# Kernel optimization log

Hardware: AMD Instinct MI355X
Metric: run time of the kernel (lower is better)

Reference implementation:

```python
import jax, jax.numpy as jnp
import numpy as np

N, D, H = 4096, 1024, 16
DK = D // H

def setup_inputs() -> dict:
    key = jax.random.key(0)
    k1, k2 = jax.random.split(key)
    X = jax.random.normal(k1, (N, D), dtype=jnp.float32)
    # torch nn.Linear(D, 2D, bias=False): weight [2D, D]; y = x @ W.T. Store as [D, 2D].
    Wqkv = jax.random.normal(k2, (D, 2 * D), dtype=jnp.float32) * (1.0 / np.sqrt(D))
    return {"X": X, "Wqkv": Wqkv}

def reference(X, Wqkv):
    n = X.shape[0]
    proj = X @ Wqkv                      # [N, 2D]
    qk, v = jnp.split(proj, 2, axis=-1)  # each [N, D]
    qk = qk.reshape(n, H, DK)
    v = v.reshape(n, H, DK)
    scale = DK ** 0.5
    scores = jnp.einsum('nhd,mhd->hnm', qk, qk) / scale  # [H, N, N], Q == K
    att = jax.nn.softmax(scores, axis=-1)
    out = jnp.einsum('hnm,mhd->nhd', att, v)              # [N, H, DK]
    return out.reshape(n, D)
```

## Files before the change

### kernel.cpp

```cpp
#include <hip/hip_runtime.h>

typedef unsigned short u16;
typedef unsigned int u32;
typedef __bf16 bf16x8 __attribute__((ext_vector_type(8)));
typedef float f32x4 __attribute__((ext_vector_type(4)));
typedef float f32x16 __attribute__((ext_vector_type(16)));
typedef int i32x2 __attribute__((ext_vector_type(2)));
typedef unsigned int u32x4 __attribute__((ext_vector_type(4)));

#define N_TOK 4096
#define DMODEL 1024
#define NH 16
#define DKH 64

__device__ inline u16 f2bf(float f){
  unsigned u = __float_as_uint(f);
  u += 0x7fffu + ((u >> 16) & 1u);
  return (u16)(u >> 16);
}

__device__ inline float fexp2(float x){ return __builtin_amdgcn_exp2f(x); }

__global__ __launch_bounds__(256) void k_convX(const float* __restrict__ X, u16* __restrict__ Xb){
  int i = blockIdx.x*256 + threadIdx.x;
  const float4 v = reinterpret_cast<const float4*>(X)[i];
  ushort4 o; o.x=f2bf(v.x); o.y=f2bf(v.y); o.z=f2bf(v.z); o.w=f2bf(v.w);
  reinterpret_cast<ushort4*>(Xb)[i] = o;
}

__global__ __launch_bounds__(256) void k_convW(const float* __restrict__ W, u16* __restrict__ Wt){
  __shared__ float tile[64][65];
  const int bn = blockIdx.x*64;
  const int bk = blockIdx.y*64;
  const int t = threadIdx.x;
  const int c4 = (t & 15)*4;
  const int r  = t >> 4;
  #pragma unroll
  for (int i=0;i<4;i++){
    int k = r + i*16;
    const float4 v = *reinterpret_cast<const float4*>(&W[(size_t)(bk+k)*2048 + bn + c4]);
    tile[k][c4+0]=v.x; tile[k][c4+1]=v.y; tile[k][c4+2]=v.z; tile[k][c4+3]=v.w;
  }
  __syncthreads();
  #pragma unroll
  for (int i=0;i<4;i++){
    int n = r + i*16;
    ushort4 o;
    o.x = f2bf(tile[c4+0][n]);
    o.y = f2bf(tile[c4+1][n]);
    o.z = f2bf(tile[c4+2][n]);
    o.w = f2bf(tile[c4+3][n]);
    *reinterpret_cast<ushort4*>(&Wt[(size_t)(bn+n)*1024 + bk + c4]) = o;
  }
}

__global__ __launch_bounds__(256) void k_gemm(const u16* __restrict__ A, const u16* __restrict__ B,
                                              u16* __restrict__ kf_g, u16* __restrict__ vf_g){
  __shared__ alignas(16) u16 As[128*64];
  __shared__ alignas(16) u16 Bs[128*64];
  const int bm = blockIdx.y*128, bn = blockIdx.x*128;
  const int tid = threadIdx.x, wid = tid>>6, lane = tid&63;
  const int wr = wid>>1, wc = wid&1;
  const int lr = lane&15, lg = lane>>4;
  f32x4 acc[4][4] = {};

  for (int kk=0; kk<DMODEL; kk+=64){
    __syncthreads();
    #pragma unroll
    for (int i=0;i<4;i++){
      const int chunk = (wid*4+i)*64 + lane;
      const int row = chunk>>3, koc = chunk&7;
      const int swz = koc ^ (row&7);
      const u16* ga = A + (size_t)(bm+row)*DMODEL + kk + swz*8;
      const u16* gb = B + (size_t)(bn+row)*DMODEL + kk + swz*8;
      __builtin_amdgcn_global_load_lds((const __attribute__((address_space(1))) void*)ga,
          (__attribute__((address_space(3))) void*)(&As[(size_t)chunk*8]), 16, 0, 0);
      __builtin_amdgcn_global_load_lds((const __attribute__((address_space(1))) void*)gb,
          (__attribute__((address_space(3))) void*)(&Bs[(size_t)chunk*8]), 16, 0, 0);
    }
    asm volatile("s_waitcnt vmcnt(0)" ::: "memory");
    __syncthreads();
    #pragma unroll
    for (int ks=0; ks<2; ks++){
      bf16x8 af[4], bfr[4];
      #pragma unroll
      for (int m=0;m<4;m++){
        const int row = wr*64+m*16+lr, cr = ks*4+lg;
        af[m] = *reinterpret_cast<const bf16x8*>(&As[(size_t)(row*8 + (cr ^ (row&7)))*8]);
      }
      #pragma unroll
      for (int n=0;n<4;n++){
        const int row = wc*64+n*16+lr, cr = ks*4+lg;
        bfr[n] = *reinterpret_cast<const bf16x8*>(&Bs[(size_t)(row*8 + (cr ^ (row&7)))*8]);
      }
      #pragma unroll
      for (int m=0;m<4;m++)
        #pragma unroll
        for (int n=0;n<4;n++)
          acc[m][n] = __builtin_amdgcn_mfma_f32_16x16x32_bf16(af[m], bfr[n], acc[m][n], 0,0,0);
    }
  }

  #pragma unroll
  for (int m=0;m<4;m++){
    const int row0 = bm + wr*64 + m*16 + lg*4;
    #pragma unroll
    for (int n=0;n<4;n++){
      const int c = bn + wc*64 + n*16 + lr;
      if (c < DMODEL){
        const int hh = c>>6, d = c&63;
        const size_t base = ((size_t)hh*512 + (size_t)(row0>>5)*4 + (d>>4))*512;
        #pragma unroll
        for (int r=0;r<4;r++){
          const int row = row0 + r;
          kf_g[base + (size_t)(((row&31) | (((d>>3)&1)<<5)))*8 + (d&7)] = f2bf(acc[m][n][r]);
        }
      } else {
        const int cc = c - DMODEL; const int hh = cc>>6, d = cc&63;
        const size_t base = (((size_t)hh*64 + (row0>>6))*8 + (d>>5)*4 + ((row0>>4)&3))*512
                          + (size_t)(((d&31) | (((row0>>3)&1)<<5)))*8 + (row0&7);
        ushort4 o;
        o.x = f2bf(acc[m][n][0]); o.y = f2bf(acc[m][n][1]);
        o.z = f2bf(acc[m][n][2]); o.w = f2bf(acc[m][n][3]);
        *reinterpret_cast<ushort4*>(&vf_g[base]) = o;
      }
    }
  }
}

__device__ inline bf16x8 scale_bf8(bf16x8 v, float s){
  u32x4 w = __builtin_bit_cast(u32x4, v);
  u32x4 r;
  #pragma unroll
  for (int i=0;i<4;i++){
    float lo = __uint_as_float(w[i] << 16) * s;
    float hi = __uint_as_float(w[i] & 0xffff0000u) * s;
    u32 p;
    asm("v_cvt_pk_bf16_f32 %0, %1, %2" : "=v"(p) : "v"(lo), "v"(hi));
    r[i] = p;
  }
  return __builtin_bit_cast(bf16x8, r);
}

__global__ __launch_bounds__(256,3) void k_attn(const u16* __restrict__ kf_g, const u16* __restrict__ vf_g,
                                                float* __restrict__ out){
  __shared__ float comb[3][64][17];
  const int bid  = blockIdx.x;
  const int xcd  = bid & 7;
  const int slot = bid >> 3;
  const int h    = (xcd<<1) | (slot>>7);
  const int qt   = slot & 127;
  const int wid  = threadIdx.x >> 6;
  const int lane = threadIdx.x & 63;
  const int ql   = lane & 31;
  const int q0   = qt*32;
  const u16* __restrict__ Kfh = kf_g + (size_t)h*262144;
  const u16* __restrict__ Vfh = vf_g + (size_t)h*262144;
  const float SC = 0.18033688011112042f;

  bf16x8 qb[4];
  #pragma unroll
  for (int ds=0; ds<4; ds++){
    bf16x8 raw = *reinterpret_cast<const bf16x8*>(&Kfh[(size_t)((q0>>5)*4 + ds)*512 + lane*8]);
    qb[ds] = scale_bf8(raw, SC);
  }

  f32x16 o0 = {}, o1 = {};
  float lp = 0.f;
  const int kb = wid*1024;

  for (int s=0; s<32; ++s){
    const int kt = kb + s*32;
    const u16* kp = Kfh + ((size_t)(kt>>5)*4)*512 + lane*8;
    bf16x8 kf0 = *reinterpret_cast<const bf16x8*>(kp);
    bf16x8 kf1 = *reinterpret_cast<const bf16x8*>(kp + 512);
    bf16x8 kf2 = *reinterpret_cast<const bf16x8*>(kp + 1024);
    bf16x8 kf3 = *reinterpret_cast<const bf16x8*>(kp + 1536);
    const u16* vb = Vfh + ((size_t)((kt>>6)*8 + (s&1)*2))*512 + lane*8;
    bf16x8 va0 = *reinterpret_cast<const bf16x8*>(vb);
    bf16x8 va1 = *reinterpret_cast<const bf16x8*>(vb + 512);
    bf16x8 vb0 = *reinterpret_cast<const bf16x8*>(vb + 4*512);
    bf16x8 vb1 = *reinterpret_cast<const bf16x8*>(vb + 5*512);

    f32x16 p = {};
    p = __builtin_amdgcn_mfma_f32_32x32x16_bf16(kf0, qb[0], p, 0,0,0);
    p = __builtin_amdgcn_mfma_f32_32x32x16_bf16(kf1, qb[1], p, 0,0,0);
    p = __builtin_amdgcn_mfma_f32_32x32x16_bf16(kf2, qb[2], p, 0,0,0);
    p = __builtin_amdgcn_mfma_f32_32x32x16_bf16(kf3, qb[3], p, 0,0,0);

    #pragma unroll
    for (int c=0; c<16; c++) p[c] = fexp2(p[c]);
    {
      float r0 = ((p[0]+p[1])+(p[2]+p[3])) + ((p[4]+p[5])+(p[6]+p[7]));
      float r1 = ((p[8]+p[9])+(p[10]+p[11])) + ((p[12]+p[13])+(p[14]+p[15]));
      lp += r0+r1;
    }

    u32 pk[8];
    #pragma unroll
    for (int c2=0; c2<8; c2++){
      u32 a;
      asm("v_cvt_pk_bf16_f32 %0, %1, %2" : "=v"(a) : "v"(p[2*c2]), "v"(p[2*c2+1]));
      pk[c2] = a;
    }
    #pragma unroll
    for (int t2=0; t2<2; t2++){
      const int base = 4*t2;
      i32x2 r0s = __builtin_amdgcn_permlane32_swap((int)pk[base+0], (int)pk[base+2], false, false);
      i32x2 r1s = __builtin_amdgcn_permlane32_swap((int)pk[base+1], (int)pk[base+3], false, false);
      u32x4 w; w[0] = (u32)r0s[0]; w[1] = (u32)r1s[0]; w[2] = (u32)r0s[1]; w[3] = (u32)r1s[1];
      bf16x8 bt = __builtin_bit_cast(bf16x8, w);
      o0 = __builtin_amdgcn_mfma_f32_32x32x16_bf16(t2 ? va1 : va0, bt, o0, 0,0,0);
      o1 = __builtin_amdgcn_mfma_f32_32x32x16_bf16(t2 ? vb1 : vb0, bt, o1, 0,0,0);
    }
  }

  lp += __shfl_xor(lp, 32, 64);

  if (wid){
    float* c = &comb[wid-1][lane][0];
    #pragma unroll
    for (int g=0; g<16; g++) c[g] = o0[g];
    c[16] = lp;
  }
  __syncthreads();
  if (!wid){
    #pragma unroll
    for (int w=0; w<3; w++){
      const float* c = &comb[w][lane][0];
      #pragma unroll
      for (int g=0; g<16; g++) o0[g] += c[g];
      lp += c[16];
    }
  }
  __syncthreads();
  if (wid){
    float* c = &comb[wid-1][lane][0];
    #pragma unroll
    for (int g=0; g<16; g++) c[g] = o1[g];
  }
  __syncthreads();
  if (!wid){
    #pragma unroll
    for (int w=0; w<3; w++){
      const float* c = &comb[w][lane][0];
      #pragma unroll
      for (int g=0; g<16; g++) o1[g] += c[g];
    }
    const int hi = lane >> 5;
    const float inv = 1.f / lp;
    float* orow = out + (size_t)(q0 + ql)*DMODEL + h*DKH;
    #pragma unroll
    for (int g=0; g<4; g++){
      float4 s0, s1;
      s0.x = o0[4*g+0]*inv; s0.y = o0[4*g+1]*inv; s0.z = o0[4*g+2]*inv; s0.w = o0[4*g+3]*inv;
      s1.x = o1[4*g+0]*inv; s1.y = o1[4*g+1]*inv; s1.z = o1[4*g+2]*inv; s1.w = o1[4*g+3]*inv;
      *reinterpret_cast<float4*>(&orow[      8*g + 4*hi]) = s0;
      *reinterpret_cast<float4*>(&orow[32 +  8*g + 4*hi]) = s1;
    }
  }
}

extern "C" void kernel_launch(void* const* d_in, const int* in_sizes, int n_in,
                              void* d_out, int out_size, void* d_ws, size_t ws_size,
                              hipStream_t stream) {
  const float* X = (const float*)d_in[0];
  const float* W = (const float*)d_in[1];
  float* out = (float*)d_out;
  u16* Xb = (u16*)d_ws;
  u16* Wt = Xb + (size_t)N_TOK*DMODEL;
  u16* Kf = Wt + (size_t)2*DMODEL*DMODEL;
  u16* Vf = Kf + (size_t)N_TOK*DMODEL;

  k_convX<<<dim3(4096), dim3(256), 0, stream>>>(X, Xb);
  k_convW<<<dim3(32,16), dim3(256), 0, stream>>>(W, Wt);
  k_gemm <<<dim3(16,32), dim3(256), 0, stream>>>(Xb, Wt, Kf, Vf);
  k_attn <<<dim3(2048), dim3(256), 0, stream>>>(Kf, Vf, out);
}
```

Baseline: 133.4 us.

## Share K/V tiles across four query warps via double-buffered LDS staging

The attention kernel changes from splitting keys across four warps (each holding the same 32 queries, then reducing through shared memory) to giving each warp its own 32 queries. K/V tiles are loaded once per block into double-buffered LDS with global_load_lds and reused by all four warps, and the cross-warp reduction is removed. The intent is to cut global/L2 traffic for K and V by a factor of four and to overlap loads with compute. In exchange the grid shrinks to 512 blocks, occupancy drops (launch bounds 2, 64KB LDS), and two barriers per tile are added.

New measurement: 118.2 us. 1.13x faster.

```diff
diff --git a/kernel.cpp b/kernel.cpp
--- a/kernel.cpp
+++ b/kernel.cpp
@@ -142,18 +142,18 @@
   return __builtin_bit_cast(bf16x8, r);
 }
 
-__global__ __launch_bounds__(256,3) void k_attn(const u16* __restrict__ kf_g, const u16* __restrict__ vf_g,
+__global__ __launch_bounds__(256,2) void k_attn(const u16* __restrict__ kf_g, const u16* __restrict__ vf_g,
                                                 float* __restrict__ out){
-  __shared__ float comb[3][64][17];
+  __shared__ alignas(16) u16 stg[2][16384];
   const int bid  = blockIdx.x;
   const int xcd  = bid & 7;
   const int slot = bid >> 3;
-  const int h    = (xcd<<1) | (slot>>7);
-  const int qt   = slot & 127;
+  const int h    = (xcd<<1) | (slot>>5);
+  const int qt   = slot & 31;
   const int wid  = threadIdx.x >> 6;
   const int lane = threadIdx.x & 63;
   const int ql   = lane & 31;
-  const int q0   = qt*32;
+  const int q0   = qt*128 + wid*32;
   const u16* __restrict__ Kfh = kf_g + (size_t)h*262144;
   const u16* __restrict__ Vfh = vf_g + (size_t)h*262144;
   const float SC = 0.18033688011112042f;
@@ -167,97 +167,88 @@
 
   f32x16 o0 = {}, o1 = {};
   float lp = 0.f;
-  const int kb = wid*1024;
-
-  for (int s=0; s<32; ++s){
-    const int kt = kb + s*32;
-    const u16* kp = Kfh + ((size_t)(kt>>5)*4)*512 + lane*8;
-    bf16x8 kf0 = *reinterpret_cast<const bf16x8*>(kp);
-    bf16x8 kf1 = *reinterpret_cast<const bf16x8*>(kp + 512);
-    bf16x8 kf2 = *reinterpret_cast<const bf16x8*>(kp + 1024);
-    bf16x8 kf3 = *reinterpret_cast<const bf16x8*>(kp + 1536);
-    const u16* vb = Vfh + ((size_t)((kt>>6)*8 + (s&1)*2))*512 + lane*8;
-    bf16x8 va0 = *reinterpret_cast<const bf16x8*>(vb);
-    bf16x8 va1 = *reinterpret_cast<const bf16x8*>(vb + 512);
-    bf16x8 vb0 = *reinterpret_cast<const bf16x8*>(vb + 4*512);
-    bf16x8 vb1 = *reinterpret_cast<const bf16x8*>(vb + 5*512);
-
-    f32x16 p = {};
-    p = __builtin_amdgcn_mfma_f32_32x32x16_bf16(kf0, qb[0], p, 0,0,0);
-    p = __builtin_amdgcn_mfma_f32_32x32x16_bf16(kf1, qb[1], p, 0,0,0);
-    p = __builtin_amdgcn_mfma_f32_32x32x16_bf16(kf2, qb[2], p, 0,0,0);
-    p = __builtin_amdgcn_mfma_f32_32x32x16_bf16(kf3, qb[3], p, 0,0,0);
-
-    #pragma unroll
-    for (int c=0; c<16; c++) p[c] = fexp2(p[c]);
-    {
-      float r0 = ((p[0]+p[1])+(p[2]+p[3])) + ((p[4]+p[5])+(p[6]+p[7]));
-      float r1 = ((p[8]+p[9])+(p[10]+p[11])) + ((p[12]+p[13])+(p[14]+p[15]));
-      lp += r0+r1;
-    }
-
-    u32 pk[8];
-    #pragma unroll
-    for (int c2=0; c2<8; c2++){
-      u32 a;
-      asm("v_cvt_pk_bf16_f32 %0, %1, %2" : "=v"(a) : "v"(p[2*c2]), "v"(p[2*c2+1]));
-      pk[c2] = a;
-    }
-    #pragma unroll
-    for (int t2=0; t2<2; t2++){
-      const int base = 4*t2;
-      i32x2 r0s = __builtin_amdgcn_permlane32_swap((int)pk[base+0], (int)pk[base+2], false, false);
-      i32x2 r1s = __builtin_amdgcn_permlane32_swap((int)pk[base+1], (int)pk[base+3], false, false);
-      u32x4 w; w[0] = (u32)r0s[0]; w[1] = (u32)r1s[0]; w[2] = (u32)r0s[1]; w[3] = (u32)r1s[1];
-      bf16x8 bt = __builtin_bit_cast(bf16x8, w);
-      o0 = __builtin_amdgcn_mfma_f32_32x32x16_bf16(t2 ? va1 : va0, bt, o0, 0,0,0);
-      o1 = __builtin_amdgcn_mfma_f32_32x32x16_bf16(t2 ? vb1 : vb0, bt, o1, 0,0,0);
-    }
+
+  auto stage = [&](int buf, int t){
+    #pragma unroll
+    for (int i=0; i<8; i++){
+      const int c = wid + i*4;
+      const u16* src = (c < 16)
+        ? Kfh + ((size_t)(t*16 + c))*512 + lane*8
+        : Vfh + ((size_t)(t*16 + c - 16))*512 + lane*8;
+      __builtin_amdgcn_global_load_lds((const __attribute__((address_space(1))) void*)src,
+          (__attribute__((address_space(3))) void*)(&stg[buf][(size_t)c*512]), 16, 0, 0);
+    }
+  };
+
+  stage(0, 0);
+  int cur = 0;
+  for (int t=0; t<32; ++t){
+    asm volatile("s_waitcnt vmcnt(0)" ::: "memory");
+    __syncthreads();
+    if (t < 31) stage(cur^1, t+1);
+
+    const u16* kb = &stg[cur][0];
+    #pragma unroll
+    for (int ss=0; ss<4; ++ss){
+      bf16x8 kf0 = *reinterpret_cast<const bf16x8*>(&kb[(size_t)(ss*4+0)*512 + lane*8]);
+      bf16x8 kf1 = *reinterpret_cast<const bf16x8*>(&kb[(size_t)(ss*4+1)*512 + lane*8]);
+      bf16x8 kf2 = *reinterpret_cast<const bf16x8*>(&kb[(size_t)(ss*4+2)*512 + lane*8]);
+      bf16x8 kf3 = *reinterpret_cast<const bf16x8*>(&kb[(size_t)(ss*4+3)*512 + lane*8]);
+
+      f32x16 p = {};
+      p = __builtin_amdgcn_mfma_f32_32x32x16_bf16(kf0, qb[0], p, 0,0,0);
+      p = __builtin_amdgcn_mfma_f32_32x32x16_bf16(kf1, qb[1], p, 0,0,0);
+      p = __builtin_amdgcn_mfma_f32_32x32x16_bf16(kf2, qb[2], p, 0,0,0);
+      p = __builtin_amdgcn_mfma_f32_32x32x16_bf16(kf3, qb[3], p, 0,0,0);
+
+      const int vbase = 8192 + ((ss>>1)*8 + (ss&1)*2)*512;
+      bf16x8 va0 = *reinterpret_cast<const bf16x8*>(&kb[(size_t)vbase          + lane*8]);
+      bf16x8 va1 = *reinterpret_cast<const bf16x8*>(&kb[(size_t)vbase +   512  + lane*8]);
+      bf16x8 vb0 = *reinterpret_cast<const bf16x8*>(&kb[(size_t)vbase + 4*512  + lane*8]);
+      bf16x8 vb1 = *reinterpret_cast<const bf16x8*>(&kb[(size_t)vbase + 5*512  + lane*8]);
+
+      #pragma unroll
+      for (int c=0; c<16; c++) p[c] = fexp2(p[c]);
+      {
+        float r0 = ((p[0]+p[1])+(p[2]+p[3])) + ((p[4]+p[5])+(p[6]+p[7]));
+        float r1 = ((p[8]+p[9])+(p[10]+p[11])) + ((p[12]+p[13])+(p[14]+p[15]));
+        lp += r0+r1;
+      }
+
+      u32 pk[8];
+      #pragma unroll
+      for (int c2=0; c2<8; c2++){
+        u32 a;
+        asm("v_cvt_pk_bf16_f32 %0, %1, %2" : "=v"(a) : "v"(p[2*c2]), "v"(p[2*c2+1]));
+        pk[c2] = a;
+      }
+      #pragma unroll
+      for (int t2=0; t2<2; t2++){
+        const int base = 4*t2;
+        i32x2 r0s = __builtin_amdgcn_permlane32_swap((int)pk[base+0], (int)pk[base+2], false, false);
+        i32x2 r1s = __builtin_amdgcn_permlane32_swap((int)pk[base+1], (int)pk[base+3], false, false);
+        u32x4 w; w[0] = (u32)r0s[0]; w[1] = (u32)r1s[0]; w[2] = (u32)r0s[1]; w[3] = (u32)r1s[1];
+        bf16x8 bt = __builtin_bit_cast(bf16x8, w);
+        o0 = __builtin_amdgcn_mfma_f32_32x32x16_bf16(t2 ? va1 : va0, bt, o0, 0,0,0);
+        o1 = __builtin_amdgcn_mfma_f32_32x32x16_bf16(t2 ? vb1 : vb0, bt, o1, 0,0,0);
+      }
+    }
+    __syncthreads();
+    cur ^= 1;
   }
 
   lp += __shfl_xor(lp, 32, 64);
 
-  if (wid){
-    float* c = &comb[wid-1][lane][0];
-    #pragma unroll
-    for (int g=0; g<16; g++) c[g] = o0[g];
-    c[16] = lp;
-  }
-  __syncthreads();
-  if (!wid){
-    #pragma unroll
-    for (int w=0; w<3; w++){
-      const float* c = &comb[w][lane][0];
-      #pragma unroll
-      for (int g=0; g<16; g++) o0[g] += c[g];
-      lp += c[16];
-    }
-  }
-  __syncthreads();
-  if (wid){
-    float* c = &comb[wid-1][lane][0];
-    #pragma unroll
-    for (int g=0; g<16; g++) c[g] = o1[g];
-  }
-  __syncthreads();
-  if (!wid){
-    #pragma unroll
-    for (int w=0; w<3; w++){
-      const float* c = &comb[w][lane][0];
-      #pragma unroll
-      for (int g=0; g<16; g++) o1[g] += c[g];
-    }
-    const int hi = lane >> 5;
-    const float inv = 1.f / lp;
-    float* orow = out + (size_t)(q0 + ql)*DMODEL + h*DKH;
-    #pragma unroll
-    for (int g=0; g<4; g++){
-      float4 s0, s1;
-      s0.x = o0[4*g+0]*inv; s0.y = o0[4*g+1]*inv; s0.z = o0[4*g+2]*inv; s0.w = o0[4*g+3]*inv;
-      s1.x = o1[4*g+0]*inv; s1.y = o1[4*g+1]*inv; s1.z = o1[4*g+2]*inv; s1.w = o1[4*g+3]*inv;
-      *reinterpret_cast<float4*>(&orow[      8*g + 4*hi]) = s0;
-      *reinterpret_cast<float4*>(&orow[32 +  8*g + 4*hi]) = s1;
-    }
+  const int hi = lane >> 5;
+  const float inv = 1.f / lp;
+  float* orow = out + (size_t)(q0 + ql)*DMODEL + h*DKH;
+  #pragma unroll
+  for (int g=0; g<4; g++){
+    float4 s0, s1;
+    s0.x = o0[4*g+0]*inv; s0.y = o0[4*g+1]*inv; s0.z = o0[4*g+2]*inv; s0.w = o0[4*g+3]*inv;
+    s1.x = o1[4*g+0]*inv; s1.y = o1[4*g+1]*inv; s1.z = o1[4*g+2]*inv; s1.w = o1[4*g+3]*inv;
+    *reinterpret_cast<float4*>(&orow[      8*g + 4*hi]) = s0;
+    *reinterpret_cast<float4*>(&orow[32 +  8*g + 4*hi]) = s1;
   }
 }
 
@@ -275,5 +266,5 @@
   k_convX<<<dim3(4096), dim3(256), 0, stream>>>(X, Xb);
   k_convW<<<dim3(32,16), dim3(256), 0, stream>>>(W, Wt);
   k_gemm <<<dim3(16,32), dim3(256), 0, stream>>>(Xb, Wt, Kf, Vf);
-  k_attn <<<dim3(2048), dim3(256), 0, stream>>>(Kf, Vf, out);
-}
+  k_attn <<<dim3(512), dim3(256), 0, stream>>>(Kf, Vf, out);
+}
```
